# Performance work log

Hardware: AMD Instinct MI355X
Metric: run time of the kernel (lower is better)

Reference implementation:

```python
import jax, jax.numpy as jnp
import numpy as np

D_MODEL, D_STATE, D_CONV, EXPAND = 1024, 16, 4, 2
D_INNER = EXPAND * D_MODEL            # 2048
DT_RANK = (D_MODEL + 15) // 16        # 64
B, L = 2, 2048


def setup_inputs() -> dict:
    key = jax.random.key(0)
    ks = jax.random.split(key, 10)
    s = 0.02
    x = jax.random.normal(ks[0], (B, L, D_MODEL), dtype=jnp.float32)
    W_in = jax.random.normal(ks[1], (2 * D_INNER, D_MODEL), dtype=jnp.float32) * s
    conv_w = jax.random.normal(ks[2], (D_INNER, D_CONV), dtype=jnp.float32) * s
    conv_b = jnp.zeros((D_INNER,), dtype=jnp.float32)
    W_xproj = jax.random.normal(ks[3], (DT_RANK + 2 * D_STATE, D_INNER), dtype=jnp.float32) * s
    W_dtproj = jax.random.normal(ks[4], (D_INNER, DT_RANK), dtype=jnp.float32) * s
    dt_bias = jax.random.uniform(ks[5], (D_INNER,), dtype=jnp.float32, minval=-4.0, maxval=-2.0)
    # S4D-real init: A_log = log(1..d_state) per channel
    A_log = jnp.log(jnp.broadcast_to(jnp.arange(1, D_STATE + 1, dtype=jnp.float32), (D_INNER, D_STATE)))
    D = jnp.ones((D_INNER,), dtype=jnp.float32)
    W_out = jax.random.normal(ks[6], (D_MODEL, D_INNER), dtype=jnp.float32) * s
    return dict(x=x, W_in=W_in, conv_w=conv_w, conv_b=conv_b, W_xproj=W_xproj,
                W_dtproj=W_dtproj, dt_bias=dt_bias, A_log=A_log, D=D, W_out=W_out)


def _mamba_forward(x, W_in, conv_w, conv_b, W_xproj, W_dtproj, dt_bias, A_log, D, W_out):
    # in_proj: (B,L,d_model) -> (B,L,2*d_inner)
    xz = jnp.einsum('bld,ed->ble', x, W_in)
    u, z = jnp.split(xz, 2, axis=-1)                      # (B,L,Di) each
    # depthwise causal conv over time
    u_t = jnp.swapaxes(u, 1, 2)                           # (B,Di,L)
    u_c = jax.lax.conv_general_dilated(
        u_t, conv_w[:, None, :], window_strides=(1,), padding=[(D_CONV - 1, 0)],
        feature_group_count=D_INNER, dimension_numbers=('NCH', 'OIH', 'NCH'))
    u_c = jax.nn.silu(u_c + conv_b[None, :, None])
    u_c = jnp.swapaxes(u_c, 1, 2)                         # (B,L,Di)
    # x_proj -> dt, B_ssm, C_ssm
    x_dbl = jnp.einsum('bld,ed->ble', u_c, W_xproj)
    dt, B_ssm, C_ssm = jnp.split(x_dbl, [DT_RANK, DT_RANK + D_STATE], axis=-1)
    delta = jax.nn.softplus(jnp.einsum('blr,dr->bld', dt, W_dtproj) + dt_bias)  # (B,L,Di)
    A = -jnp.exp(A_log)                                   # (Di,Ds)

    def step(h, inp):
        d_t, b_t, c_t, u_t = inp                          # (B,Di),(B,Ds),(B,Ds),(B,Di)
        dA = jnp.exp(d_t[..., None] * A)                  # (B,Di,Ds)
        dBu = d_t[..., None] * b_t[:, None, :] * u_t[..., None]
        h = dA * h + dBu
        y = jnp.einsum('bds,bs->bd', h, c_t)
        return h, y

    h0 = jnp.zeros((B, D_INNER, D_STATE), dtype=x.dtype)
    xs = (jnp.swapaxes(delta, 0, 1), jnp.swapaxes(B_ssm, 0, 1),
          jnp.swapaxes(C_ssm, 0, 1), jnp.swapaxes(u_c, 0, 1))
    _, ys = jax.lax.scan(step, h0, xs)                    # (L,B,Di)
    y = jnp.swapaxes(ys, 0, 1) + u_c * D                  # skip term D*u
    y = y * jax.nn.silu(z)                                # gate
    return jnp.einsum('bld,ed->ble', y, W_out)            # (B,L,d_model)


def reference(x, W_in, conv_w, conv_b, W_xproj, W_dtproj, dt_bias, A_log, D, W_out):
    return _mamba_forward(x, W_in, conv_w, conv_b, W_xproj, W_dtproj, dt_bias, A_log, D, W_out)
```

## Files before the change

### kernel.cpp

```cpp
#include <hip/hip_runtime.h>
#include <cstdint>
#include <cstddef>

constexpr int Bc = 2, Lc = 2048, DM = 1024, DI = 2048, DS = 16, DR = 64, NX = 96;
constexpr int BL = Bc * Lc;
constexpr int NC = 32, CH = 64;
constexpr int BDS = Bc * DI * DS;
constexpr int NSK = 8;
constexpr float LOG2E = 1.44269504f;

typedef __attribute__((ext_vector_type(8))) short bf16x8;
typedef __attribute__((ext_vector_type(4))) float f32x4;
typedef unsigned short u16;

__device__ __forceinline__ u16 f2b(float f) {
  uint32_t u = __float_as_uint(f);
  return (u16)((u + 0x7FFFu + ((u >> 16) & 1u)) >> 16);
}
__device__ __forceinline__ float b2f(u16 h) {
  return __uint_as_float(((uint32_t)h) << 16);
}

__global__ __launch_bounds__(256) void cvt_hilo(
    const float* __restrict__ in, u16* __restrict__ hi, u16* __restrict__ lo,
    int n4) {
  int i = blockIdx.x * 256 + threadIdx.x;
  if (i >= n4) return;
  float4 v = reinterpret_cast<const float4*>(in)[i];
  ushort4 H, L;
  H.x = f2b(v.x); L.x = f2b(v.x - b2f(H.x));
  H.y = f2b(v.y); L.y = f2b(v.y - b2f(H.y));
  H.z = f2b(v.z); L.z = f2b(v.z - b2f(H.z));
  H.w = f2b(v.w); L.w = f2b(v.w - b2f(H.w));
  reinterpret_cast<ushort4*>(hi)[i] = H;
  reinterpret_cast<ushort4*>(lo)[i] = L;
}

__global__ __launch_bounds__(256) void cvt_pad_wx(
    const float* __restrict__ w, u16* __restrict__ hi, u16* __restrict__ lo) {
  int i = blockIdx.x * 256 + threadIdx.x;
  int f = i * 4;
  int row = f >> 11;
  ushort4 H, L;
  H.x = H.y = H.z = H.w = 0; L = H;
  if (row < 96) {
    float4 v = *reinterpret_cast<const float4*>(&w[f]);
    H.x = f2b(v.x); L.x = f2b(v.x - b2f(H.x));
    H.y = f2b(v.y); L.y = f2b(v.y - b2f(H.y));
    H.z = f2b(v.z); L.z = f2b(v.z - b2f(H.z));
    H.w = f2b(v.w); L.w = f2b(v.w - b2f(H.w));
  }
  reinterpret_cast<ushort4*>(hi)[i] = H;
  reinterpret_cast<ushort4*>(lo)[i] = L;
}

__device__ __forceinline__ void stage_tile(
    const u16* __restrict__ g, u16* lds, int row0, int ld, int k0,
    int w, int lane) {
  #pragma unroll
  for (int i = 0; i < 2; ++i) {
    const int base = w * 1024 + i * 8192;
    const int o = base + lane * 16;
    const int row = o >> 7;
    const int sl = ((o >> 4) & 7) ^ (row & 7);
    const u16* src = g + (size_t)(row0 + row) * ld + (k0 + sl * 8);
    __builtin_amdgcn_global_load_lds(
        (const __attribute__((address_space(1))) unsigned int*)src,
        (__attribute__((address_space(3))) unsigned int*)(lds + base / 2),
        16, 0, 0);
  }
}

__device__ __forceinline__ void stage4(
    const u16* __restrict__ Ah, const u16* __restrict__ Al,
    const u16* __restrict__ Bh, const u16* __restrict__ Bl,
    u16* buf , int bm, int bn, int lda, int ldb,
    int k0, int w, int lane) {
  stage_tile(Ah, buf + 0 * 8192, bm, lda, k0, w, lane);
  stage_tile(Al, buf + 1 * 8192, bm, lda, k0, w, lane);
  stage_tile(Bh, buf + 2 * 8192, bn, ldb, k0, w, lane);
  stage_tile(Bl, buf + 3 * 8192, bn, ldb, k0, w, lane);
}

__device__ __forceinline__ bf16x8 ld_frag(const u16* plane, int rowbase,
                                          int kk, int lane) {
  const int row = rowbase + (lane & 15);
  const int kb = ((kk << 2) | (lane >> 4)) ^ (row & 7);
  return *reinterpret_cast<const bf16x8*>(
      reinterpret_cast<const char*>(plane) + row * 128 + kb * 16);
}

template<int EPI>
__global__ __launch_bounds__(512) void gemm_mfma(
    const u16* __restrict__ Ah, const u16* __restrict__ Al,
    const u16* __restrict__ Bh, const u16* __restrict__ Bl,
    const float* __restrict__ bias, float* __restrict__ C,
    int M, int N, int kEff, int lda, int ldb, int ldc,
    size_t cSplitStride) {
  __shared__ __align__(16) u16 lds[2][4][8192];
  const int tid = threadIdx.x;
  const int lane = tid & 63, w = tid >> 6;
  const int wr = w >> 1, wc = w & 1;
  const int bm = blockIdx.x * 128, bn = blockIdx.y * 128;
  const int sk = blockIdx.z;
  Ah += (size_t)sk * kEff; Al += (size_t)sk * kEff;
  Bh += (size_t)sk * kEff; Bl += (size_t)sk * kEff;
  C  += (size_t)sk * cSplitStride;

  f32x4 acc[2][4] = {};
  const int nt = kEff >> 6;

  stage4(Ah, Al, Bh, Bl, &lds[0][0][0], bm, bn, lda, ldb, 0, w, lane);
  __syncthreads();

  int cur = 0;
  for (int t = 0; t < nt; ++t) {
    if (t + 1 < nt)
      stage4(Ah, Al, Bh, Bl, &lds[cur ^ 1][0][0], bm, bn, lda, ldb,
             (t + 1) * 64, w, lane);

    const u16* Lb = &lds[cur][0][0];
    #pragma unroll
    for (int kk = 0; kk < 2; ++kk) {
      bf16x8 ah[2], al[2], bh[4], bl[4];
      #pragma unroll
      for (int m = 0; m < 2; ++m) {
        ah[m] = ld_frag(Lb + 0 * 8192, wr * 32 + m * 16, kk, lane);
        al[m] = ld_frag(Lb + 1 * 8192, wr * 32 + m * 16, kk, lane);
      }
      #pragma unroll
      for (int n = 0; n < 4; ++n) {
        bh[n] = ld_frag(Lb + 2 * 8192, wc * 64 + n * 16, kk, lane);
        bl[n] = ld_frag(Lb + 3 * 8192, wc * 64 + n * 16, kk, lane);
      }
      __builtin_amdgcn_s_setprio(1);
      #pragma unroll
      for (int m = 0; m < 2; ++m)
        #pragma unroll
        for (int n = 0; n < 4; ++n)
          acc[m][n] = __builtin_amdgcn_mfma_f32_16x16x32_bf16(ah[m], bh[n], acc[m][n], 0, 0, 0);
      #pragma unroll
      for (int m = 0; m < 2; ++m)
        #pragma unroll
        for (int n = 0; n < 4; ++n)
          acc[m][n] = __builtin_amdgcn_mfma_f32_16x16x32_bf16(ah[m], bl[n], acc[m][n], 0, 0, 0);
      #pragma unroll
      for (int m = 0; m < 2; ++m)
        #pragma unroll
        for (int n = 0; n < 4; ++n)
          acc[m][n] = __builtin_amdgcn_mfma_f32_16x16x32_bf16(al[m], bh[n], acc[m][n], 0, 0, 0);
      __builtin_amdgcn_s_setprio(0);
    }
    __syncthreads();
    cur ^= 1;
  }

  const int rbase = (lane >> 4) * 4;
  const int cidx = lane & 15;
  #pragma unroll
  for (int m = 0; m < 2; ++m) {
    int grow0 = bm + wr * 32 + m * 16 + rbase;
    #pragma unroll
    for (int n = 0; n < 4; ++n) {
      int gcol = bn + wc * 64 + n * 16 + cidx;
      if (gcol < N) {
        #pragma unroll
        for (int r = 0; r < 4; ++r) {
          float v = acc[m][n][r];
          if (EPI == 1) {
            v += bias[gcol];
            v = fmaxf(v, 0.f) + log1pf(expf(-fabsf(v)));
          }
          C[(size_t)(grow0 + r) * ldc + gcol] = v;
        }
      }
    }
  }
}

__global__ __launch_bounds__(256) void xproj_reduce(
    const float* __restrict__ pbuf, float* __restrict__ xdbl,
    u16* __restrict__ xdh, u16* __restrict__ xdl) {
  int i = blockIdx.x * 256 + threadIdx.x;
  const float4* p = reinterpret_cast<const float4*>(pbuf);
  float4 s = p[i];
  #pragma unroll
  for (int sk = 1; sk < NSK; ++sk) {
    float4 v = p[(size_t)sk * (BL * NX / 4) + i];
    s.x += v.x; s.y += v.y; s.z += v.z; s.w += v.w;
  }
  reinterpret_cast<float4*>(xdbl)[i] = s;
  ushort4 H, L;
  H.x = f2b(s.x); L.x = f2b(s.x - b2f(H.x));
  H.y = f2b(s.y); L.y = f2b(s.y - b2f(H.y));
  H.z = f2b(s.z); L.z = f2b(s.z - b2f(H.z));
  H.w = f2b(s.w); L.w = f2b(s.w - b2f(H.w));
  reinterpret_cast<ushort4*>(xdh)[i] = H;
  reinterpret_cast<ushort4*>(xdl)[i] = L;
}

__global__ __launch_bounds__(256) void conv_silu4(
    const float* __restrict__ xz, const float* __restrict__ w,
    const float* __restrict__ bias, u16* __restrict__ uch,
    u16* __restrict__ ucl) {
  int i = blockIdx.x * 256 + threadIdx.x;
  int d4 = (i << 2) & (DI - 1);
  int bl = i >> 9;
  int b  = bl >> 11;
  int l  = bl & (Lc - 1);
  const float4* wrow = reinterpret_cast<const float4*>(&w[d4 * 4]);
  float4 w0 = wrow[0], w1 = wrow[1], w2 = wrow[2], w3 = wrow[3];
  float4 a = *reinterpret_cast<const float4*>(&bias[d4]);
  #pragma unroll
  for (int k = 0; k < 4; ++k) {
    int ls = l - 3 + k;
    if (ls >= 0) {
      float4 xv = *reinterpret_cast<const float4*>(
          &xz[((size_t)(b * Lc + ls)) * (2 * DI) + d4]);
      a.x = fmaf(xv.x, (&w0.x)[k], a.x);
      a.y = fmaf(xv.y, (&w1.x)[k], a.y);
      a.z = fmaf(xv.z, (&w2.x)[k], a.z);
      a.w = fmaf(xv.w, (&w3.x)[k], a.w);
    }
  }
  a.x = a.x * __frcp_rn(1.f + __expf(-a.x));
  a.y = a.y * __frcp_rn(1.f + __expf(-a.y));
  a.z = a.z * __frcp_rn(1.f + __expf(-a.z));
  a.w = a.w * __frcp_rn(1.f + __expf(-a.w));
  ushort4 H, L;
  H.x = f2b(a.x); L.x = f2b(a.x - b2f(H.x));
  H.y = f2b(a.y); L.y = f2b(a.y - b2f(H.y));
  H.z = f2b(a.z); L.z = f2b(a.z - b2f(H.z));
  H.w = f2b(a.w); L.w = f2b(a.w - b2f(H.w));
  reinterpret_cast<ushort4*>(uch)[i] = H;
  reinterpret_cast<ushort4*>(ucl)[i] = L;
}

__global__ __launch_bounds__(256) void scan_chunk_local(
    const float* __restrict__ delta, const u16* __restrict__ uch,
    const u16* __restrict__ ucl, const float* __restrict__ xdbl,
    const float* __restrict__ A_log, float* __restrict__ Pa,
    float* __restrict__ hA) {
  const int t = blockIdx.x * 256 + threadIdx.x;
  const int d = t & (DI - 1);
  const int b = (t >> 11) & (Bc - 1);
  const int c = t >> 12;
  const int bd = (b << 11) | d;

  float Av2[DS];
  {
    const float4* ap = reinterpret_cast<const float4*>(&A_log[(size_t)d * DS]);
    #pragma unroll
    for (int q = 0; q < 4; ++q) {
      float4 a = ap[q];
      Av2[4*q+0] = -LOG2E * __expf(a.x);
      Av2[4*q+1] = -LOG2E * __expf(a.y);
      Av2[4*q+2] = -LOG2E * __expf(a.z);
      Av2[4*q+3] = -LOG2E * __expf(a.w);
    }
  }
  const size_t rowbase = (size_t)(b * Lc + c * CH);
  const float* dp  = delta + rowbase * DI + d;
  const u16*   uhp = uch   + rowbase * DI + d;
  const u16*   ulp = ucl   + rowbase * DI + d;
  const float4* xp = reinterpret_cast<const float4*>(xdbl + rowbase * NX + DR);

  float h[DS] = {};
  float S = 0.f;
  float dt = dp[0];
  float ut = b2f(uhp[0]) + b2f(ulp[0]);
  float4 B0 = xp[0], B1 = xp[1], B2 = xp[2], B3 = xp[3];

  for (int l = 0; l < CH; ++l) {
    const int ln = (l + 1 < CH) ? l + 1 : l;
    float dtn = dp[ln * DI];
    float utn = b2f(uhp[ln * DI]) + b2f(ulp[ln * DI]);
    const float4* xn = xp + ln * (NX / 4);
    float4 B0n = xn[0], B1n = xn[1], B2n = xn[2], B3n = xn[3];

    float Bs[16];
    *reinterpret_cast<float4*>(&Bs[0])  = B0;
    *reinterpret_cast<float4*>(&Bs[4])  = B1;
    *reinterpret_cast<float4*>(&Bs[8])  = B2;
    *reinterpret_cast<float4*>(&Bs[12]) = B3;
    const float dtu = dt * ut;
    S += dt;
    #pragma unroll
    for (int s = 0; s < DS; ++s) {
      float dA = exp2f(dt * Av2[s]);
      h[s] = fmaf(dA, h[s], dtu * Bs[s]);
    }
    dt = dtn; ut = utn; B0 = B0n; B1 = B1n; B2 = B2n; B3 = B3n;
  }

  float4* Pp = reinterpret_cast<float4*>(&Pa[(size_t)c * BDS + (size_t)bd * DS]);
  float4* Hp = reinterpret_cast<float4*>(&hA[(size_t)c * BDS + (size_t)bd * DS]);
  #pragma unroll
  for (int q = 0; q < 4; ++q) {
    float4 pv, hv;
    pv.x = exp2f(Av2[4*q+0] * S); pv.y = exp2f(Av2[4*q+1] * S);
    pv.z = exp2f(Av2[4*q+2] * S); pv.w = exp2f(Av2[4*q+3] * S);
    hv.x = h[4*q+0]; hv.y = h[4*q+1]; hv.z = h[4*q+2]; hv.w = h[4*q+3];
    Pp[q] = pv; Hp[q] = hv;
  }
}

__global__ __launch_bounds__(256) void scan_chunk_carry(
    float* Pa_h0, const float* __restrict__ hA) {
  const int t = blockIdx.x * 256 + threadIdx.x;
  float pa[NC], ha[NC];
  #pragma unroll
  for (int c = 0; c < NC; ++c) {
    pa[c] = Pa_h0[(size_t)c * BDS + t];
    ha[c] = hA[(size_t)c * BDS + t];
  }
  float h = 0.f;
  #pragma unroll
  for (int c = 0; c < NC; ++c) {
    Pa_h0[(size_t)c * BDS + t] = h;
    h = fmaf(pa[c], h, ha[c]);
  }
}

__global__ __launch_bounds__(256) void scan_chunk_final(
    const float* __restrict__ delta, const u16* uch, const u16* ucl,
    const float* __restrict__ xdbl, const float* __restrict__ xz,
    const float* __restrict__ A_log, const float* __restrict__ Dv,
    const float* __restrict__ h0, u16* yh, u16* yl) {
  const int t = blockIdx.x * 256 + threadIdx.x;
  const int d = t & (DI - 1);
  const int b = (t >> 11) & (Bc - 1);
  const int c = t >> 12;
  const int bd = (b << 11) | d;

  float Av2[DS];
  {
    const float4* ap = reinterpret_cast<const float4*>(&A_log[(size_t)d * DS]);
    #pragma unroll
    for (int q = 0; q < 4; ++q) {
      float4 a = ap[q];
      Av2[4*q+0] = -LOG2E * __expf(a.x);
      Av2[4*q+1] = -LOG2E * __expf(a.y);
      Av2[4*q+2] = -LOG2E * __expf(a.z);
      Av2[4*q+3] = -LOG2E * __expf(a.w);
    }
  }
  const float Dd = Dv[d];
  float h[DS];
  {
    const float4* hp = reinterpret_cast<const float4*>(&h0[(size_t)c * BDS + (size_t)bd * DS]);
    #pragma unroll
    for (int q = 0; q < 4; ++q) {
      float4 hv = hp[q];
      h[4*q+0] = hv.x; h[4*q+1] = hv.y; h[4*q+2] = hv.z; h[4*q+3] = hv.w;
    }
  }
  const size_t rowbase = (size_t)(b * Lc + c * CH);
  const float* dp  = delta + rowbase * DI + d;
  const u16*   uhp = uch   + rowbase * DI + d;
  const u16*   ulp = ucl   + rowbase * DI + d;
  const float* zp  = xz    + rowbase * (2 * DI) + DI + d;
  const float4* xp = reinterpret_cast<const float4*>(xdbl + rowbase * NX + DR);
  u16* yhp = yh + rowbase * DI + d;
  u16* ylp = yl + rowbase * DI + d;

  float dt = dp[0];
  float ut = b2f(uhp[0]) + b2f(ulp[0]);
  float zt = zp[0];
  float4 B0 = xp[0], B1 = xp[1], B2 = xp[2], B3 = xp[3];
  float4 C0 = xp[4], C1 = xp[5], C2 = xp[6], C3 = xp[7];

  for (int l = 0; l < CH; ++l) {
    const int ln = (l + 1 < CH) ? l + 1 : l;
    float dtn = dp[ln * DI];
    float utn = b2f(uhp[ln * DI]) + b2f(ulp[ln * DI]);
    float ztn = zp[ln * (2 * DI)];
    const float4* xn = xp + ln * (NX / 4);
    float4 B0n = xn[0], B1n = xn[1], B2n = xn[2], B3n = xn[3];
    float4 C0n = xn[4], C1n = xn[5], C2n = xn[6], C3n = xn[7];

    float Bs[16], Cs[16];
    *reinterpret_cast<float4*>(&Bs[0])  = B0;
    *reinterpret_cast<float4*>(&Bs[4])  = B1;
    *reinterpret_cast<float4*>(&Bs[8])  = B2;
    *reinterpret_cast<float4*>(&Bs[12]) = B3;
    *reinterpret_cast<float4*>(&Cs[0])  = C0;
    *reinterpret_cast<float4*>(&Cs[4])  = C1;
    *reinterpret_cast<float4*>(&Cs[8])  = C2;
    *reinterpret_cast<float4*>(&Cs[12]) = C3;
    const float dtu = dt * ut;
    float y0 = 0.f, y1 = 0.f;
    #pragma unroll
    for (int s = 0; s < DS; ++s) {
      float dA = exp2f(dt * Av2[s]);
      h[s] = fmaf(dA, h[s], dtu * Bs[s]);
      if (s & 1) y1 = fmaf(h[s], Cs[s], y1);
      else       y0 = fmaf(h[s], Cs[s], y0);
    }
    float gate = zt * __frcp_rn(1.f + exp2f(-LOG2E * zt));
    float y = (y0 + y1 + Dd * ut) * gate;
    u16 hh = f2b(y);
    yhp[l * DI] = hh;
    ylp[l * DI] = f2b(y - b2f(hh));

    dt = dtn; ut = utn; zt = ztn;
    B0 = B0n; B1 = B1n; B2 = B2n; B3 = B3n;
    C0 = C0n; C1 = C1n; C2 = C2n; C3 = C3n;
  }
}

extern "C" void kernel_launch(void* const* d_in, const int* in_sizes, int n_in,
                              void* d_out, int out_size, void* d_ws, size_t ws_size,
                              hipStream_t stream) {
  const float* x        = (const float*)d_in[0];
  const float* W_in     = (const float*)d_in[1];
  const float* conv_w   = (const float*)d_in[2];
  const float* conv_b   = (const float*)d_in[3];
  const float* W_xproj  = (const float*)d_in[4];
  const float* W_dtproj = (const float*)d_in[5];
  const float* dt_bias  = (const float*)d_in[6];
  const float* A_log    = (const float*)d_in[7];
  const float* Dv       = (const float*)d_in[8];
  const float* W_out    = (const float*)d_in[9];
  float* out = (float*)d_out;

  char* W = (char*)d_ws;
  size_t off = 0;
  float* xz  = (float*)(W + off);  off += (size_t)BL * 4096 * 4;
  size_t delta_off = off;
  u16* xh   = (u16*)(W + off);     off += (size_t)BL * DM * 2;
  u16* xl   = (u16*)(W + off);     off += (size_t)BL * DM * 2;
  u16* Wih  = (u16*)(W + off);     off += (size_t)(2 * DI) * DM * 2;
  u16* Wil  = (u16*)(W + off);     off += (size_t)(2 * DI) * DM * 2;
  float* delta = (float*)(W + delta_off);
  u16* uch  = (u16*)(W + off);     off += (size_t)BL * DI * 2;
  u16* ucl  = (u16*)(W + off);     off += (size_t)BL * DI * 2;
  u16* Wxh  = (u16*)(W + off);     off += (size_t)128 * DI * 2;
  u16* Wxl  = (u16*)(W + off);     off += (size_t)128 * DI * 2;
  float* xdbl = (float*)(W + off); off += (size_t)BL * NX * 4;
  u16* xdh  = (u16*)(W + off);     off += (size_t)BL * NX * 2;
  u16* xdl  = (u16*)(W + off);     off += (size_t)BL * NX * 2;
  u16* Wdh  = (u16*)(W + off);     off += (size_t)DI * DR * 2;
  u16* Wdl  = (u16*)(W + off);     off += (size_t)DI * DR * 2;
  u16* Woh  = (u16*)(W + off);     off += (size_t)DM * DI * 2;
  u16* Wol  = (u16*)(W + off);     off += (size_t)DM * DI * 2;
  float* Pa = (float*)(W + off);   off += (size_t)NC * BDS * 4;
  float* hA = (float*)(W + off);   off += (size_t)NC * BDS * 4;
  float* h0 = Pa;
  float* pbuf = Pa;
  u16* yh = uch;
  u16* yl = ucl;

  cvt_hilo<<<(BL * DM / 4 + 255) / 256, 256, 0, stream>>>(x, xh, xl, BL * DM / 4);
  cvt_hilo<<<(2 * DI * DM / 4 + 255) / 256, 256, 0, stream>>>(W_in, Wih, Wil, 2 * DI * DM / 4);
  cvt_pad_wx<<<(128 * DI / 4) / 256, 256, 0, stream>>>(W_xproj, Wxh, Wxl);
  cvt_hilo<<<(DI * DR / 4 + 255) / 256, 256, 0, stream>>>(W_dtproj, Wdh, Wdl, DI * DR / 4);
  cvt_hilo<<<(DM * DI / 4 + 255) / 256, 256, 0, stream>>>(W_out, Woh, Wol, DM * DI / 4);

  gemm_mfma<0><<<dim3(BL / 128, (2 * DI) / 128, 1), 512, 0, stream>>>(
      xh, xl, Wih, Wil, nullptr, xz, BL, 2 * DI, DM, DM, DM, 2 * DI, 0);

  conv_silu4<<<(BL * DI / 4) / 256, 256, 0, stream>>>(xz, conv_w, conv_b, uch, ucl);

  gemm_mfma<0><<<dim3(BL / 128, 1, NSK), 512, 0, stream>>>(
      uch, ucl, Wxh, Wxl, nullptr, pbuf, BL, NX, DI / NSK, DI, DI, NX,
      (size_t)BL * NX);

  xproj_reduce<<<(BL * NX / 4) / 256, 256, 0, stream>>>(pbuf, xdbl, xdh, xdl);

  gemm_mfma<1><<<dim3(BL / 128, DI / 128, 1), 512, 0, stream>>>(
      xdh, xdl, Wdh, Wdl, dt_bias, delta, BL, DI, DR, NX, DR, DI, 0);

  scan_chunk_local<<<(Bc * DI * NC) / 256, 256, 0, stream>>>(
      delta, uch, ucl, xdbl, A_log, Pa, hA);
  scan_chunk_carry<<<BDS / 256, 256, 0, stream>>>(Pa, hA);
  scan_chunk_final<<<(Bc * DI * NC) / 256, 256, 0, stream>>>(
      delta, uch, ucl, xdbl, xz, A_log, Dv, h0, yh, yl);

  gemm_mfma<0><<<dim3(BL / 128, DM / 128, 1), 512, 0, stream>>>(
      yh, yl, Woh, Wol, nullptr, out, BL, DM, DI, DI, DI, DM, 0);
}
```

Before: 437.6 us.

## Restructure split-bf16 GEMM to 256 threads, K=32 tiles, and deeper async prefetch

The GEMM now runs 4 waves per block, each computing a 64x64 subtile (4x4 accumulators), with K-steps of 32 and a halved LDS footprint using a 4-way XOR swizzle. Loads are issued two stages ahead and the sync uses explicit vmcnt waits plus raw barriers instead of __syncthreads, aiming to overlap global-to-LDS copies with MFMA work. The five fp32-to-hi/lo conversion kernels are merged into one launch to cut launch overhead. Risks include higher register pressure from the larger accumulator set and vmcnt counts that must exactly match the number of outstanding loads.

```diff
diff --git a/kernel.cpp b/kernel.cpp
--- a/kernel.cpp
+++ b/kernel.cpp
@@ -21,37 +21,40 @@
   return __uint_as_float(((uint32_t)h) << 16);
 }
 
-__global__ __launch_bounds__(256) void cvt_hilo(
-    const float* __restrict__ in, u16* __restrict__ hi, u16* __restrict__ lo,
-    int n4) {
+constexpr int S0 = BL * DM / 4;
+constexpr int S1 = 2 * DI * DM / 4;
+constexpr int S2 = 128 * DI / 4;
+constexpr int S3 = DI * DR / 4;
+constexpr int S4 = DM * DI / 4;
+constexpr int CVT_TOT = S0 + S1 + S2 + S3 + S4;
+
+__global__ __launch_bounds__(256) void cvt_all(
+    const float* __restrict__ x, const float* __restrict__ W_in,
+    const float* __restrict__ W_xproj, const float* __restrict__ W_dtproj,
+    const float* __restrict__ W_out,
+    u16* __restrict__ xh, u16* __restrict__ xl,
+    u16* __restrict__ Wih, u16* __restrict__ Wil,
+    u16* __restrict__ Wxh, u16* __restrict__ Wxl,
+    u16* __restrict__ Wdh, u16* __restrict__ Wdl,
+    u16* __restrict__ Woh, u16* __restrict__ Wol) {
   int i = blockIdx.x * 256 + threadIdx.x;
-  if (i >= n4) return;
-  float4 v = reinterpret_cast<const float4*>(in)[i];
+  if (i >= CVT_TOT) return;
+  const float* src; u16 *dh, *dl; int idx; bool zero = false;
+  if (i < S0)                { src = x;        dh = xh;  dl = xl;  idx = i; }
+  else if (i < S0+S1)        { src = W_in;     dh = Wih; dl = Wil; idx = i - S0; }
+  else if (i < S0+S1+S2)     { src = W_xproj;  dh = Wxh; dl = Wxl; idx = i - S0 - S1;
+                               if (((idx * 4) >> 11) >= 96) zero = true; }
+  else if (i < S0+S1+S2+S3)  { src = W_dtproj; dh = Wdh; dl = Wdl; idx = i - S0 - S1 - S2; }
+  else                       { src = W_out;    dh = Woh; dl = Wol; idx = i - S0 - S1 - S2 - S3; }
+  float4 v = zero ? make_float4(0.f, 0.f, 0.f, 0.f)
+                  : reinterpret_cast<const float4*>(src)[idx];
   ushort4 H, L;
   H.x = f2b(v.x); L.x = f2b(v.x - b2f(H.x));
   H.y = f2b(v.y); L.y = f2b(v.y - b2f(H.y));
   H.z = f2b(v.z); L.z = f2b(v.z - b2f(H.z));
   H.w = f2b(v.w); L.w = f2b(v.w - b2f(H.w));
-  reinterpret_cast<ushort4*>(hi)[i] = H;
-  reinterpret_cast<ushort4*>(lo)[i] = L;
-}
-
-__global__ __launch_bounds__(256) void cvt_pad_wx(
-    const float* __restrict__ w, u16* __restrict__ hi, u16* __restrict__ lo) {
-  int i = blockIdx.x * 256 + threadIdx.x;
-  int f = i * 4;
-  int row = f >> 11;
-  ushort4 H, L;
-  H.x = H.y = H.z = H.w = 0; L = H;
-  if (row < 96) {
-    float4 v = *reinterpret_cast<const float4*>(&w[f]);
-    H.x = f2b(v.x); L.x = f2b(v.x - b2f(H.x));
-    H.y = f2b(v.y); L.y = f2b(v.y - b2f(H.y));
-    H.z = f2b(v.z); L.z = f2b(v.z - b2f(H.z));
-    H.w = f2b(v.w); L.w = f2b(v.w - b2f(H.w));
-  }
-  reinterpret_cast<ushort4*>(hi)[i] = H;
-  reinterpret_cast<ushort4*>(lo)[i] = L;
+  reinterpret_cast<ushort4*>(dh)[idx] = H;
+  reinterpret_cast<ushort4*>(dl)[idx] = L;
 }
 
 __device__ __forceinline__ void stage_tile(
@@ -59,10 +62,10 @@
     int w, int lane) {
   #pragma unroll
   for (int i = 0; i < 2; ++i) {
-    const int base = w * 1024 + i * 8192;
+    const int base = w * 1024 + i * 4096;
     const int o = base + lane * 16;
-    const int row = o >> 7;
-    const int sl = ((o >> 4) & 7) ^ (row & 7);
+    const int row = o >> 6;
+    const int sl = ((o >> 4) & 3) ^ ((row >> 1) & 3);
     const u16* src = g + (size_t)(row0 + row) * ld + (k0 + sl * 8);
     __builtin_amdgcn_global_load_lds(
         (const __attribute__((address_space(1))) unsigned int*)src,
@@ -76,28 +79,27 @@
     const u16* __restrict__ Bh, const u16* __restrict__ Bl,
     u16* buf , int bm, int bn, int lda, int ldb,
     int k0, int w, int lane) {
-  stage_tile(Ah, buf + 0 * 8192, bm, lda, k0, w, lane);
-  stage_tile(Al, buf + 1 * 8192, bm, lda, k0, w, lane);
-  stage_tile(Bh, buf + 2 * 8192, bn, ldb, k0, w, lane);
-  stage_tile(Bl, buf + 3 * 8192, bn, ldb, k0, w, lane);
-}
-
-__device__ __forceinline__ bf16x8 ld_frag(const u16* plane, int rowbase,
-                                          int kk, int lane) {
+  stage_tile(Ah, buf + 0 * 4096, bm, lda, k0, w, lane);
+  stage_tile(Al, buf + 1 * 4096, bm, lda, k0, w, lane);
+  stage_tile(Bh, buf + 2 * 4096, bn, ldb, k0, w, lane);
+  stage_tile(Bl, buf + 3 * 4096, bn, ldb, k0, w, lane);
+}
+
+__device__ __forceinline__ bf16x8 ld_frag(const u16* plane, int rowbase, int lane) {
   const int row = rowbase + (lane & 15);
-  const int kb = ((kk << 2) | (lane >> 4)) ^ (row & 7);
+  const int kb = (lane >> 4) ^ ((row >> 1) & 3);
   return *reinterpret_cast<const bf16x8*>(
-      reinterpret_cast<const char*>(plane) + row * 128 + kb * 16);
+      reinterpret_cast<const char*>(plane) + row * 64 + kb * 16);
 }
 
 template<int EPI>
-__global__ __launch_bounds__(512) void gemm_mfma(
+__global__ __launch_bounds__(256) void gemm_mfma(
     const u16* __restrict__ Ah, const u16* __restrict__ Al,
     const u16* __restrict__ Bh, const u16* __restrict__ Bl,
     const float* __restrict__ bias, float* __restrict__ C,
     int M, int N, int kEff, int lda, int ldb, int ldc,
     size_t cSplitStride) {
-  __shared__ __align__(16) u16 lds[2][4][8192];
+  __shared__ __align__(16) u16 lds[2][4][4096];
   const int tid = threadIdx.x;
   const int lane = tid & 63, w = tid >> 6;
   const int wr = w >> 1, wc = w & 1;
@@ -107,59 +109,59 @@
   Bh += (size_t)sk * kEff; Bl += (size_t)sk * kEff;
   C  += (size_t)sk * cSplitStride;
 
-  f32x4 acc[2][4] = {};
-  const int nt = kEff >> 6;
+  f32x4 acc[4][4] = {};
+  const int nt = kEff >> 5;
 
   stage4(Ah, Al, Bh, Bl, &lds[0][0][0], bm, bn, lda, ldb, 0, w, lane);
-  __syncthreads();
+  stage4(Ah, Al, Bh, Bl, &lds[1][0][0], bm, bn, lda, ldb, 32, w, lane);
 
   int cur = 0;
   for (int t = 0; t < nt; ++t) {
-    if (t + 1 < nt)
-      stage4(Ah, Al, Bh, Bl, &lds[cur ^ 1][0][0], bm, bn, lda, ldb,
-             (t + 1) * 64, w, lane);
+    if (t + 1 < nt) asm volatile("s_waitcnt vmcnt(8)" ::: "memory");
+    else            asm volatile("s_waitcnt vmcnt(0)" ::: "memory");
+    __builtin_amdgcn_s_barrier();
 
     const u16* Lb = &lds[cur][0][0];
-    #pragma unroll
-    for (int kk = 0; kk < 2; ++kk) {
-      bf16x8 ah[2], al[2], bh[4], bl[4];
+    bf16x8 ah[4], al[4], bh[4], bl[4];
+    #pragma unroll
+    for (int m = 0; m < 4; ++m) {
+      ah[m] = ld_frag(Lb + 0 * 4096, wr * 64 + m * 16, lane);
+      al[m] = ld_frag(Lb + 1 * 4096, wr * 64 + m * 16, lane);
+    }
+    #pragma unroll
+    for (int n = 0; n < 4; ++n) {
+      bh[n] = ld_frag(Lb + 2 * 4096, wc * 64 + n * 16, lane);
+      bl[n] = ld_frag(Lb + 3 * 4096, wc * 64 + n * 16, lane);
+    }
+    __builtin_amdgcn_s_setprio(1);
+    #pragma unroll
+    for (int m = 0; m < 4; ++m)
       #pragma unroll
-      for (int m = 0; m < 2; ++m) {
-        ah[m] = ld_frag(Lb + 0 * 8192, wr * 32 + m * 16, kk, lane);
-        al[m] = ld_frag(Lb + 1 * 8192, wr * 32 + m * 16, kk, lane);
-      }
+      for (int n = 0; n < 4; ++n)
+        acc[m][n] = __builtin_amdgcn_mfma_f32_16x16x32_bf16(ah[m], bh[n], acc[m][n], 0, 0, 0);
+    #pragma unroll
+    for (int m = 0; m < 4; ++m)
       #pragma unroll
-      for (int n = 0; n < 4; ++n) {
-        bh[n] = ld_frag(Lb + 2 * 8192, wc * 64 + n * 16, kk, lane);
-        bl[n] = ld_frag(Lb + 3 * 8192, wc * 64 + n * 16, kk, lane);
-      }
-      __builtin_amdgcn_s_setprio(1);
+      for (int n = 0; n < 4; ++n)
+        acc[m][n] = __builtin_amdgcn_mfma_f32_16x16x32_bf16(ah[m], bl[n], acc[m][n], 0, 0, 0);
+    #pragma unroll
+    for (int m = 0; m < 4; ++m)
       #pragma unroll
-      for (int m = 0; m < 2; ++m)
-        #pragma unroll
-        for (int n = 0; n < 4; ++n)
-          acc[m][n] = __builtin_amdgcn_mfma_f32_16x16x32_bf16(ah[m], bh[n], acc[m][n], 0, 0, 0);
-      #pragma unroll
-      for (int m = 0; m < 2; ++m)
-        #pragma unroll
-        for (int n = 0; n < 4; ++n)
-          acc[m][n] = __builtin_amdgcn_mfma_f32_16x16x32_bf16(ah[m], bl[n], acc[m][n], 0, 0, 0);
-      #pragma unroll
-      for (int m = 0; m < 2; ++m)
-        #pragma unroll
-        for (int n = 0; n < 4; ++n)
-          acc[m][n] = __builtin_amdgcn_mfma_f32_16x16x32_bf16(al[m], bh[n], acc[m][n], 0, 0, 0);
-      __builtin_amdgcn_s_setprio(0);
-    }
-    __syncthreads();
+      for (int n = 0; n < 4; ++n)
+        acc[m][n] = __builtin_amdgcn_mfma_f32_16x16x32_bf16(al[m], bh[n], acc[m][n], 0, 0, 0);
+    __builtin_amdgcn_s_setprio(0);
+    __builtin_amdgcn_s_barrier();
+    if (t + 2 < nt)
+      stage4(Ah, Al, Bh, Bl, &lds[cur][0][0], bm, bn, lda, ldb,
+             (t + 2) * 32, w, lane);
     cur ^= 1;
   }
 
   const int rbase = (lane >> 4) * 4;
   const int cidx = lane & 15;
   #pragma unroll
-  for (int m = 0; m < 2; ++m) {
-    int grow0 = bm + wr * 32 + m * 16 + rbase;
+  for (int m = 0; m < 4; ++m) {
+    int grow0 = bm + wr * 64 + m * 16 + rbase;
     #pragma unroll
     for (int n = 0; n < 4; ++n) {
       int gcol = bn + wc * 64 + n * 16 + cidx;
@@ -451,24 +453,22 @@
   u16* yh = uch;
   u16* yl = ucl;
 
-  cvt_hilo<<<(BL * DM / 4 + 255) / 256, 256, 0, stream>>>(x, xh, xl, BL * DM / 4);
-  cvt_hilo<<<(2 * DI * DM / 4 + 255) / 256, 256, 0, stream>>>(W_in, Wih, Wil, 2 * DI * DM / 4);
-  cvt_pad_wx<<<(128 * DI / 4) / 256, 256, 0, stream>>>(W_xproj, Wxh, Wxl);
-  cvt_hilo<<<(DI * DR / 4 + 255) / 256, 256, 0, stream>>>(W_dtproj, Wdh, Wdl, DI * DR / 4);
-  cvt_hilo<<<(DM * DI / 4 + 255) / 256, 256, 0, stream>>>(W_out, Woh, Wol, DM * DI / 4);
-
-  gemm_mfma<0><<<dim3(BL / 128, (2 * DI) / 128, 1), 512, 0, stream>>>(
+  cvt_all<<<(CVT_TOT + 255) / 256, 256, 0, stream>>>(
+      x, W_in, W_xproj, W_dtproj, W_out,
+      xh, xl, Wih, Wil, Wxh, Wxl, Wdh, Wdl, Woh, Wol);
+
+  gemm_mfma<0><<<dim3(BL / 128, (2 * DI) / 128, 1), 256, 0, stream>>>(
       xh, xl, Wih, Wil, nullptr, xz, BL, 2 * DI, DM, DM, DM, 2 * DI, 0);
 
   conv_silu4<<<(BL * DI / 4) / 256, 256, 0, stream>>>(xz, conv_w, conv_b, uch, ucl);
 
-  gemm_mfma<0><<<dim3(BL / 128, 1, NSK), 512, 0, stream>>>(
+  gemm_mfma<0><<<dim3(BL / 128, 1, NSK), 256, 0, stream>>>(
       uch, ucl, Wxh, Wxl, nullptr, pbuf, BL, NX, DI / NSK, DI, DI, NX,
       (size_t)BL * NX);
 
   xproj_reduce<<<(BL * NX / 4) / 256, 256, 0, stream>>>(pbuf, xdbl, xdh, xdl);
 
-  gemm_mfma<1><<<dim3(BL / 128, DI / 128, 1), 512, 0, stream>>>(
+  gemm_mfma<1><<<dim3(BL / 128, DI / 128, 1), 256, 0, stream>>>(
       xdh, xdl, Wdh, Wdl, dt_bias, delta, BL, DI, DR, NX, DR, DI, 0);
 
   scan_chunk_local<<<(Bc * DI * NC) / 256, 256, 0, stream>>>(
@@ -477,6 +477,6 @@
   scan_chunk_final<<<(Bc * DI * NC) / 256, 256, 0, stream>>>(
       delta, uch, ucl, xdbl, xz, A_log, Dv, h0, yh, yl);
 
-  gemm_mfma<0><<<dim3(BL / 128, DM / 128, 1), 512, 0, stream>>>(
+  gemm_mfma<0><<<dim3(BL / 128, DM / 128, 1), 256, 0, stream>>>(
       yh, yl, Woh, Wol, nullptr, out, BL, DM, DI, DI, DI, DM, 0);
 }
```

After: 454.5 us. 1.04x slower.
